# Kernel optimization log

Measured on AMD Instinct MI355X. Metric: run time of the kernel, lower is better.

Reference implementation:

```python
import jax, jax.numpy as jnp
import numpy as np

N = 100000   # nodes
E = 3200000  # edges
F = 128      # in = hidden = out channels
V = 8        # virtual nodes
L = 3        # conv layers
EPS = 1e-5


def setup_inputs() -> dict:
    key = jax.random.key(0)
    ks = jax.random.split(key, 16)
    rn = lambda k, s, sc=0.05: jax.random.normal(k, s, jnp.float32) * sc
    return {
        "x": rn(ks[0], (N, F), 1.0),
        "edge_index": jax.random.randint(ks[1], (2, E), 0, N, jnp.int32),
        "vn_mask": jax.random.randint(ks[2], (V, N), 0, 2, jnp.int32).astype(bool),
        "Wc": rn(ks[3], (L, F, F)),
        "bc": rn(ks[4], (L, F)),
        "bn_g": jnp.ones((L, F), jnp.float32),
        "bn_b": jnp.zeros((L, F), jnp.float32),
        "vn_embed": rn(ks[5], (V, F)),
        "mlp_W1": rn(ks[6], (L - 1, V, F, 2 * F)),
        "mlp_b1": rn(ks[7], (L - 1, V, 2 * F)),
        "ln1_g": jnp.ones((L - 1, V, 2 * F), jnp.float32),
        "ln1_b": jnp.zeros((L - 1, V, 2 * F), jnp.float32),
        "mlp_W2": rn(ks[8], (L - 1, V, 2 * F, F)),
        "mlp_b2": rn(ks[9], (L - 1, V, F)),
        "ln2_g": jnp.ones((L - 1, V, F), jnp.float32),
        "ln2_b": jnp.zeros((L - 1, V, F), jnp.float32),
    }


def _ln(h, g, b):
    m = h.mean(-1, keepdims=True)
    v = ((h - m) ** 2).mean(-1, keepdims=True)
    return (h - m) * jax.lax.rsqrt(v + EPS) * g + b


def _bn(h, g, b):  # training-mode batch stats over nodes (dropout p=0)
    m = h.mean(0)
    v = ((h - m) ** 2).mean(0)
    return (h - m) * jax.lax.rsqrt(v + EPS) * g + b


def reference(x, edge_index, vn_mask, Wc, bc, bn_g, bn_b, vn_embed,
              mlp_W1, mlp_b1, ln1_g, ln1_b, mlp_W2, mlp_b2, ln2_g, ln2_b):
    src, dst = edge_index[0], edge_index[1]
    loops = jnp.arange(N, dtype=src.dtype)
    src_f = jnp.concatenate([src, loops])   # GCN adds self-loops
    dst_f = jnp.concatenate([dst, loops])
    deg = jax.ops.segment_sum(jnp.ones(src_f.shape[0], x.dtype), dst_f, num_segments=N)
    dinv = jnp.where(deg > 0, jax.lax.rsqrt(deg), 0.0)
    norm = dinv[src_f] * dinv[dst_f]        # sym-normalized edge weights

    def gcn(h, W, b):  # PyG GCNConv: linear -> normalized scatter-sum -> bias
        hl = h @ W
        out = jax.ops.segment_sum(hl[src_f] * norm[:, None], dst_f, num_segments=N)
        return out + b

    maskf = vn_mask.astype(x.dtype)  # [V, N]
    vn = vn_embed                    # [V, F]
    embs = [x]
    for layer in range(L):
        h = embs[layer] + vn.sum(0, keepdims=True)       # aggregation='sum'
        h = gcn(h, Wc[layer], bc[layer])
        h = _bn(h, bn_g[layer], bn_b[layer])
        if layer != L - 1:
            h = jax.nn.relu(h)
        embs.append(h)
        if layer < L - 1:
            pooled = maskf @ embs[layer]                 # per-VN global_add_pool
            tmp = pooled + vn
            h1 = jax.nn.relu(jnp.einsum('vf,vfh->vh', tmp, mlp_W1[layer]) + mlp_b1[layer])
            h1 = _ln(h1, ln1_g[layer], ln1_b[layer])
            h2 = jax.nn.relu(jnp.einsum('vh,vhf->vf', h1, mlp_W2[layer]) + mlp_b2[layer])
            vn = _ln(h2, ln2_g[layer], ln2_b[layer])
    return embs[-1]  # JK='last'
```

## Files before the change

kernel.cpp:

```cpp
#include <hip/hip_runtime.h>
#include <hip/hip_bf16.h>
#include <hip/hip_fp16.h>

#define NN 100000
#define EE 3200000
#define FF 128
#define F2 256
#define VV 8
#define LL 3
#define EPSV 1e-5f
#define NB 98

static inline int idiv(int a, int b){ return (a + b - 1) / b; }

__global__ void k_deg(const int* __restrict__ dst, int* __restrict__ edeg){
  int stride = gridDim.x * 256;
  for (int e = blockIdx.x * 256 + threadIdx.x; e < EE; e += stride)
    atomicAdd(&edeg[dst[e]], 1);
}

__global__ void k_scanA(const int* __restrict__ edeg, int* __restrict__ offs,
                        int* __restrict__ bsum, float* __restrict__ dinv){
  __shared__ int s[1024];
  int t = threadIdx.x;
  int i = blockIdx.x * 1024 + t;
  int v = (i < NN) ? edeg[i] : 0;
  if (i < NN) dinv[i] = rsqrtf((float)(v + 1));
  int x = v;
  s[t] = x; __syncthreads();
  for (int d = 1; d < 1024; d <<= 1){
    int y = (t >= d) ? s[t - d] : 0;
    __syncthreads();
    x += y; s[t] = x;
    __syncthreads();
  }
  if (i < NN) offs[i] = x - v;
  if (t == 1023) bsum[blockIdx.x] = x;
}

__global__ void k_scanB(int* __restrict__ bsum){
  __shared__ int s[128];
  int t = threadIdx.x;
  s[t] = (t < NB) ? bsum[t] : 0;
  __syncthreads();
  if (t == 0){
    int run = 0;
    for (int k = 0; k < NB; ++k){ int tmp = s[k]; s[k] = run; run += tmp; }
  }
  __syncthreads();
  if (t < NB) bsum[t] = s[t];
}

__global__ void k_scanC(int* __restrict__ offs, const int* __restrict__ bsum,
                        int* __restrict__ cursor){
  int i = blockIdx.x * 256 + threadIdx.x;
  if (i < NN){
    int o = offs[i] + bsum[i >> 10];
    offs[i] = o;
    cursor[i] = o;
  }
  if (i == 0) offs[NN] = EE;
}

__global__ void k_scatter(const int* __restrict__ src, const int* __restrict__ dst,
                          int* __restrict__ cursor, int* __restrict__ ssorted){
  int stride = gridDim.x * 256;
  for (int e = blockIdx.x * 256 + threadIdx.x; e < EE; e += stride){
    int d = dst[e];
    int pos = atomicAdd(&cursor[d], 1);
    ssorted[pos] = src[e];
  }
}

__global__ void k_maskdetect(const unsigned char* __restrict__ m, int* __restrict__ flag){
  int any = 0;
  for (int t = threadIdx.x; t < 4096; t += 256)
    if ((t & 3) && m[t]) any = 1;
  if (any) atomicOr(flag, 1);
}

__launch_bounds__(256)
__global__ void k_matmul(const float* __restrict__ in, const float* __restrict__ W,
                         const float* __restrict__ vn, const float* __restrict__ dinv,
                         const float* __restrict__ ss, int hasbn,
                         uint2* __restrict__ hlb){
  __shared__ float Ws[FF * FF];
  __shared__ float As[32 * FF];
  __shared__ float vs[FF];
  __shared__ float rv[FF];
  __shared__ float scs[FF], shs[FF];
  int tid = threadIdx.x;
  for (int t = tid; t < FF * FF; t += 256) Ws[t] = W[t];
  if (tid < FF){
    float s = 0.f;
    for (int v = 0; v < VV; ++v) s += vn[v * FF + tid];
    vs[tid] = s;
    scs[tid] = hasbn ? ss[tid] : 1.0f;
    shs[tid] = hasbn ? ss[FF + tid] : 0.0f;
  }
  __syncthreads();
  if (tid < FF){
    float a = 0.f;
    for (int k = 0; k < FF; ++k) a += vs[k] * Ws[k * FF + tid];
    rv[tid] = a;
  }
  __syncthreads();
  int g = tid >> 5;
  int c = tid & 31;
  float4 rvv = ((const float4*)rv)[c];
  for (int base = blockIdx.x * 32; base < NN; base += gridDim.x * 32){
    const float4* in4 = (const float4*)(in + (size_t)base * FF);
    for (int i = tid; i < 32 * 32; i += 256){
      float4 vv = in4[i];
      if (hasbn){
        int cq = (i & 31) * 4;
        vv.x = fmaxf(fmaf(vv.x, scs[cq + 0], shs[cq + 0]), 0.f);
        vv.y = fmaxf(fmaf(vv.y, scs[cq + 1], shs[cq + 1]), 0.f);
        vv.z = fmaxf(fmaf(vv.z, scs[cq + 2], shs[cq + 2]), 0.f);
        vv.w = fmaxf(fmaf(vv.w, scs[cq + 3], shs[cq + 3]), 0.f);
      }
      ((float4*)As)[i] = vv;
    }
    __syncthreads();
    float4 a0 = rvv, a1 = rvv, a2 = rvv, a3 = rvv;
    #pragma unroll 4
    for (int k = 0; k < FF; ++k){
      float4 wv = ((const float4*)Ws)[k * 32 + c];
      float x0 = As[(g +  0) * FF + k];
      float x1 = As[(g +  8) * FF + k];
      float x2 = As[(g + 16) * FF + k];
      float x3 = As[(g + 24) * FF + k];
      a0.x += x0 * wv.x; a0.y += x0 * wv.y; a0.z += x0 * wv.z; a0.w += x0 * wv.w;
      a1.x += x1 * wv.x; a1.y += x1 * wv.y; a1.z += x1 * wv.z; a1.w += x1 * wv.w;
      a2.x += x2 * wv.x; a2.y += x2 * wv.y; a2.z += x2 * wv.z; a2.w += x2 * wv.w;
      a3.x += x3 * wv.x; a3.y += x3 * wv.y; a3.z += x3 * wv.z; a3.w += x3 * wv.w;
    }
    #pragma unroll
    for (int rr = 0; rr < 4; ++rr){
      float4 a = (rr == 0) ? a0 : (rr == 1) ? a1 : (rr == 2) ? a2 : a3;
      int r = base + g + 8 * rr;
      float d = dinv[r];
      __half2 h01 = __floats2half2_rn(a.x * d, a.y * d);
      __half2 h23 = __floats2half2_rn(a.z * d, a.w * d);
      uint2 pk;
      pk.x = *reinterpret_cast<unsigned int*>(&h01);
      pk.y = *reinterpret_cast<unsigned int*>(&h23);
      hlb[(size_t)r * 32 + c] = pk;
    }
    __syncthreads();
  }
}

__launch_bounds__(256)
__global__ void k_gather(const unsigned int* __restrict__ hlb, const float* __restrict__ dinv,
                         const int* __restrict__ offs, const int* __restrict__ ssorted,
                         float2* __restrict__ agg2, float* __restrict__ stats){
  int tid = threadIdx.x;
  int lane = tid & 63;
  int wid = (blockIdx.x * 256 + tid) >> 6;
  int nw = (gridDim.x * 256) >> 6;
  float s0 = 0.f, s1 = 0.f, q0 = 0.f, q1 = 0.f;
  for (int n = wid; n < NN; n += nw){
    int off0 = offs[n], off1 = offs[n + 1];
    unsigned int ps = hlb[(size_t)n * 64 + lane];
    float2 acc = __half22float2(*reinterpret_cast<__half2*>(&ps));
    #pragma unroll 8
    for (int e = off0; e < off1; ++e){
      unsigned int p = hlb[(size_t)ssorted[e] * 64 + lane];
      float2 f = __half22float2(*reinterpret_cast<__half2*>(&p));
      acc.x += f.x; acc.y += f.y;
    }
    float dv = dinv[n];
    float v0 = acc.x * dv, v1 = acc.y * dv;
    agg2[(size_t)n * 64 + lane] = make_float2(v0, v1);
    s0 += v0; s1 += v1; q0 += v0 * v0; q1 += v1 * v1;
  }
  __shared__ float4 red[256];
  red[tid] = make_float4(s0, s1, q0, q1);
  __syncthreads();
  if (tid < 64){
    float4 a = red[tid], b = red[tid + 64], c = red[tid + 128], d = red[tid + 192];
    a.x += b.x + c.x + d.x; a.y += b.y + c.y + d.y;
    a.z += b.z + c.z + d.z; a.w += b.w + c.w + d.w;
    atomicAdd(&stats[2 * tid], a.x);
    atomicAdd(&stats[2 * tid + 1], a.y);
    atomicAdd(&stats[FF + 2 * tid], a.z);
    atomicAdd(&stats[FF + 2 * tid + 1], a.w);
  }
}

__global__ void k_bnfin(const float* __restrict__ stats, const float* __restrict__ g,
                        const float* __restrict__ b, float* __restrict__ ss){
  int j = threadIdx.x;
  float mean = stats[j] * (1.0f / NN);
  float var  = stats[FF + j] * (1.0f / NN) - mean * mean;
  float sc = rsqrtf(var + EPSV) * g[j];
  ss[j] = sc;
  ss[FF + j] = b[j] - mean * sc;
}

__launch_bounds__(256)
__global__ void k_bnapply(float4* __restrict__ h, const float* __restrict__ stats,
                          const float* __restrict__ g, const float* __restrict__ b){
  __shared__ float ss[2 * FF];
  int tid = threadIdx.x;
  if (tid < FF){
    float mean = stats[tid] * (1.0f / NN);
    float var  = stats[FF + tid] * (1.0f / NN) - mean * mean;
    float sc = rsqrtf(var + EPSV) * g[tid];
    ss[tid] = sc;
    ss[FF + tid] = b[tid] - mean * sc;
  }
  __syncthreads();
  int n4 = NN * FF / 4;
  int stride = gridDim.x * 256;
  for (int i = blockIdx.x * 256 + tid; i < n4; i += stride){
    int c = (i & 31) * 4;
    float4 v = h[i];
    float4 sc = *(const float4*)&ss[c];
    float4 sh = *(const float4*)&ss[FF + c];
    v.x = v.x * sc.x + sh.x;
    v.y = v.y * sc.y + sh.y;
    v.z = v.z * sc.z + sh.z;
    v.w = v.w * sc.w + sh.w;
    h[i] = v;
  }
}

__global__ void k_pool(const float* __restrict__ emb, const unsigned char* __restrict__ m8,
                       const int* __restrict__ m32, const int* __restrict__ flag,
                       const float* __restrict__ ss, int hasbn,
                       float* __restrict__ pooled){
  int isb = *flag;
  int tid = blockIdx.x * 256 + threadIdx.x;
  int j = tid & 127;
  int r = tid >> 7;
  int rs = (gridDim.x * 256) >> 7;
  float sc = hasbn ? ss[j] : 1.0f;
  float sh = hasbn ? ss[FF + j] : 0.0f;
  float acc[VV];
  #pragma unroll
  for (int v = 0; v < VV; ++v) acc[v] = 0.f;
  for (; r < NN; r += rs){
    float xv = emb[r * FF + j];
    xv = fmaf(xv, sc, sh);
    if (hasbn) xv = fmaxf(xv, 0.f);
    #pragma unroll
    for (int v = 0; v < VV; ++v){
      int mv = isb ? (int)m8[v * NN + r] : m32[v * NN + r];
      if (mv) acc[v] += xv;
    }
  }
  #pragma unroll
  for (int v = 0; v < VV; ++v) atomicAdd(&pooled[v * FF + j], acc[v]);
}

__device__ __forceinline__ float blockSum(float x, float* red, int tid){
  red[tid] = x; __syncthreads();
  #pragma unroll
  for (int s = 128; s >= 1; s >>= 1){
    if (tid < s) red[tid] += red[tid + s];
    __syncthreads();
  }
  float r = red[0];
  __syncthreads();
  return r;
}

__launch_bounds__(256)
__global__ void k_vnmlp(const float* __restrict__ pooled, const float* __restrict__ vnin,
                        const float* __restrict__ W1, const float* __restrict__ b1,
                        const float* __restrict__ g1, const float* __restrict__ bb1,
                        const float* __restrict__ W2, const float* __restrict__ b2,
                        const float* __restrict__ g2, const float* __restrict__ bb2,
                        float* __restrict__ vnout){
  int v = blockIdx.x;
  int tid = threadIdx.x;
  __shared__ float tmp_s[FF];
  __shared__ float h1_s[F2];
  __shared__ float red[256];
  if (tid < FF) tmp_s[tid] = pooled[v * FF + tid] + vnin[v * FF + tid];
  __syncthreads();
  const float* W1v = W1 + (size_t)v * FF * F2;
  float acc = b1[v * F2 + tid];
  for (int k = 0; k < FF; ++k) acc += tmp_s[k] * W1v[k * F2 + tid];
  acc = fmaxf(acc, 0.f);
  float sum = blockSum(acc, red, tid);
  float sq  = blockSum(acc * acc, red, tid);
  float mean = sum * (1.f / F2);
  float var  = sq * (1.f / F2) - mean * mean;
  float y = (acc - mean) * rsqrtf(var + EPSV) * g1[v * F2 + tid] + bb1[v * F2 + tid];
  h1_s[tid] = y;
  __syncthreads();
  const float* W2v = W2 + (size_t)v * F2 * FF;
  float h2 = 0.f;
  if (tid < FF){
    float a2 = b2[v * FF + tid];
    for (int k = 0; k < F2; ++k) a2 += h1_s[k] * W2v[k * FF + tid];
    h2 = fmaxf(a2, 0.f);
  }
  float sum2 = blockSum((tid < FF) ? h2 : 0.f, red, tid);
  float sq2  = blockSum((tid < FF) ? h2 * h2 : 0.f, red, tid);
  float mean2 = sum2 * (1.f / FF);
  float var2  = sq2 * (1.f / FF) - mean2 * mean2;
  if (tid < FF)
    vnout[v * FF + tid] = (h2 - mean2) * rsqrtf(var2 + EPSV) * g2[v * FF + tid]
                          + bb2[v * FF + tid];
}

extern "C" void kernel_launch(void* const* d_in, const int* in_sizes, int n_in,
                              void* d_out, int out_size, void* d_ws, size_t ws_size,
                              hipStream_t stream){
  const float* x        = (const float*)d_in[0];
  const int*   ei       = (const int*)d_in[1];
  const unsigned char* vmask8 = (const unsigned char*)d_in[2];
  const int*   vmask32  = (const int*)d_in[2];
  const float* Wc       = (const float*)d_in[3];
  const float* bn_g     = (const float*)d_in[5];
  const float* bn_b     = (const float*)d_in[6];
  const float* vn_embed = (const float*)d_in[7];
  const float* mlp_W1   = (const float*)d_in[8];
  const float* mlp_b1   = (const float*)d_in[9];
  const float* ln1_g    = (const float*)d_in[10];
  const float* ln1_b    = (const float*)d_in[11];
  const float* mlp_W2   = (const float*)d_in[12];
  const float* mlp_b2   = (const float*)d_in[13];
  const float* ln2_g    = (const float*)d_in[14];
  const float* ln2_b    = (const float*)d_in[15];
  float* out = (float*)d_out;

  unsigned int* hlb = (unsigned int*)d_ws;
  float* bufB    = (float*)(hlb + (size_t)NN * 64);
  int*   ssorted = (int*)(bufB + (size_t)NN * FF);
  int*   offs    = ssorted + EE;
  int*   cursor  = offs + NN + 1;
  int*   edeg    = cursor + NN;
  int*   bsum    = edeg + NN;
  float* dinv    = (float*)(bsum + 128);
  float* stats   = dinv + NN;
  float* ssA     = stats + 2 * FF;
  float* ssB     = ssA + 2 * FF;
  float* pooled  = ssB + 2 * FF;
  float* vnA     = pooled + VV * FF;
  float* vnB     = vnA + VV * FF;
  int*   mflag   = (int*)(vnB + VV * FF);

  const int* esrc = ei;
  const int* edst = ei + EE;

  hipMemsetAsync(edeg, 0, NN * sizeof(int), stream);
  k_deg<<<1024, 256, 0, stream>>>(edst, edeg);
  k_scanA<<<NB, 1024, 0, stream>>>(edeg, offs, bsum, dinv);
  k_scanB<<<1, 128, 0, stream>>>(bsum);
  k_scanC<<<idiv(NN, 256), 256, 0, stream>>>(offs, bsum, cursor);
  k_scatter<<<2048, 256, 0, stream>>>(esrc, edst, cursor, ssorted);

  hipMemsetAsync(mflag, 0, sizeof(int), stream);
  k_maskdetect<<<1, 256, 0, stream>>>(vmask8, mflag);

  const float* vncur = vn_embed;
  const float* embin = x;
  float* ssbufs[2] = {ssA, ssB};
  const float* sscur = nullptr;
  float* vnbufs[2] = {vnA, vnB};

  for (int l = 0; l < LL; ++l){
    float* agg = (l < LL - 1) ? bufB : out;
    const float* Wl = Wc + (size_t)l * FF * FF;
    int hasbn = (l > 0) ? 1 : 0;

    k_matmul<<<1024, 256, 0, stream>>>(embin, Wl, vncur, dinv, sscur, hasbn, (uint2*)hlb);

    if (l < LL - 1){
      hipMemsetAsync(pooled, 0, VV * FF * sizeof(float), stream);
      k_pool<<<1024, 256, 0, stream>>>(embin, vmask8, vmask32, mflag, sscur, hasbn, pooled);
    }

    hipMemsetAsync(stats, 0, 2 * FF * sizeof(float), stream);
    k_gather<<<2048, 256, 0, stream>>>(hlb, dinv, offs, ssorted, (float2*)agg, stats);

    if (l < LL - 1){
      k_bnfin<<<1, 128, 0, stream>>>(stats, bn_g + l * FF, bn_b + l * FF, ssbufs[l]);
      k_vnmlp<<<VV, 256, 0, stream>>>(pooled, vncur,
          mlp_W1 + (size_t)l * VV * FF * F2, mlp_b1 + (size_t)l * VV * F2,
          ln1_g + (size_t)l * VV * F2, ln1_b + (size_t)l * VV * F2,
          mlp_W2 + (size_t)l * VV * F2 * FF, mlp_b2 + (size_t)l * VV * FF,
          ln2_g + (size_t)l * VV * FF, ln2_b + (size_t)l * VV * FF,
          vnbufs[l]);
      vncur = vnbufs[l];
      sscur = ssbufs[l];
      embin = agg;
    } else {
      k_bnapply<<<1024, 256, 0, stream>>>((float4*)out, stats, bn_g + l * FF, bn_b + l * FF);
    }
  }
}
```

Before: 1.666 ms.

## Partition CSR scatter by XCD destination slice and widen gather to half-wave per node

The scatter kernel now assigns each block to one of eight destination-node slices, chosen by block index modulo 8. Each block scans all edges but only inserts those whose destination falls in its slice, so a slice's cursor atomics and ssorted writes stay on one XCD's L2. The gather kernel now handles two nodes per wavefront, with 32 lanes each loading 8-byte fp16 quads, which gives wider loads and more nodes in flight. The cost is that every scatter group reads the full edge list, eight times the index traffic, and the XCD mapping assumes round-robin block dispatch.

```diff
diff --git a/kernel.cpp b/kernel.cpp
--- a/kernel.cpp
+++ b/kernel.cpp
@@ -10,6 +10,8 @@
 #define LL 3
 #define EPSV 1e-5f
 #define NB 98
+#define NXCD 8
+#define SLICE 12500
 
 static inline int idiv(int a, int b){ return (a + b - 1) / b; }
 
@@ -64,11 +66,17 @@
 
 __global__ void k_scatter(const int* __restrict__ src, const int* __restrict__ dst,
                           int* __restrict__ cursor, int* __restrict__ ssorted){
-  int stride = gridDim.x * 256;
-  for (int e = blockIdx.x * 256 + threadIdx.x; e < EE; e += stride){
+  int grp = blockIdx.x & (NXCD - 1);
+  int lo = grp * SLICE, hi = lo + SLICE;
+  int bid = blockIdx.x >> 3;
+  int nb = gridDim.x >> 3;
+  int stride = nb * 256;
+  for (int e = bid * 256 + threadIdx.x; e < EE; e += stride){
     int d = dst[e];
-    int pos = atomicAdd(&cursor[d], 1);
-    ssorted[pos] = src[e];
+    if (d >= lo && d < hi){
+      int pos = atomicAdd(&cursor[d], 1);
+      ssorted[pos] = src[e];
+    }
   }
 }
 
@@ -152,40 +160,53 @@
 }
 
 __launch_bounds__(256)
-__global__ void k_gather(const unsigned int* __restrict__ hlb, const float* __restrict__ dinv,
+__global__ void k_gather(const uint2* __restrict__ hlb2, const float* __restrict__ dinv,
                          const int* __restrict__ offs, const int* __restrict__ ssorted,
-                         float2* __restrict__ agg2, float* __restrict__ stats){
+                         float4* __restrict__ agg4, float* __restrict__ stats){
   int tid = threadIdx.x;
-  int lane = tid & 63;
-  int wid = (blockIdx.x * 256 + tid) >> 6;
-  int nw = (gridDim.x * 256) >> 6;
-  float s0 = 0.f, s1 = 0.f, q0 = 0.f, q1 = 0.f;
-  for (int n = wid; n < NN; n += nw){
+  int ln = tid & 31;
+  int half = (tid >> 5) & 1;
+  int pair = (blockIdx.x * 256 + tid) >> 6;
+  int np = (gridDim.x * 256) >> 6;
+  float s0=0.f,s1=0.f,s2=0.f,s3=0.f, q0=0.f,q1=0.f,q2=0.f,q3=0.f;
+  for (int p = pair; p < NN / 2; p += np){
+    int n = 2 * p + half;
     int off0 = offs[n], off1 = offs[n + 1];
-    unsigned int ps = hlb[(size_t)n * 64 + lane];
-    float2 acc = __half22float2(*reinterpret_cast<__half2*>(&ps));
+    uint2 u = hlb2[(size_t)n * 32 + ln];
+    float2 a01 = __half22float2(*reinterpret_cast<__half2*>(&u.x));
+    float2 a23 = __half22float2(*reinterpret_cast<__half2*>(&u.y));
+    float acc0 = a01.x, acc1 = a01.y, acc2 = a23.x, acc3 = a23.y;
     #pragma unroll 8
     for (int e = off0; e < off1; ++e){
-      unsigned int p = hlb[(size_t)ssorted[e] * 64 + lane];
-      float2 f = __half22float2(*reinterpret_cast<__half2*>(&p));
-      acc.x += f.x; acc.y += f.y;
+      uint2 v = hlb2[(size_t)ssorted[e] * 32 + ln];
+      float2 f01 = __half22float2(*reinterpret_cast<__half2*>(&v.x));
+      float2 f23 = __half22float2(*reinterpret_cast<__half2*>(&v.y));
+      acc0 += f01.x; acc1 += f01.y; acc2 += f23.x; acc3 += f23.y;
     }
     float dv = dinv[n];
-    float v0 = acc.x * dv, v1 = acc.y * dv;
-    agg2[(size_t)n * 64 + lane] = make_float2(v0, v1);
-    s0 += v0; s1 += v1; q0 += v0 * v0; q1 += v1 * v1;
-  }
-  __shared__ float4 red[256];
-  red[tid] = make_float4(s0, s1, q0, q1);
-  __syncthreads();
-  if (tid < 64){
-    float4 a = red[tid], b = red[tid + 64], c = red[tid + 128], d = red[tid + 192];
-    a.x += b.x + c.x + d.x; a.y += b.y + c.y + d.y;
-    a.z += b.z + c.z + d.z; a.w += b.w + c.w + d.w;
-    atomicAdd(&stats[2 * tid], a.x);
-    atomicAdd(&stats[2 * tid + 1], a.y);
-    atomicAdd(&stats[FF + 2 * tid], a.z);
-    atomicAdd(&stats[FF + 2 * tid + 1], a.w);
+    float v0 = acc0*dv, v1 = acc1*dv, v2 = acc2*dv, v3 = acc3*dv;
+    agg4[(size_t)n * 32 + ln] = make_float4(v0, v1, v2, v3);
+    s0 += v0; s1 += v1; s2 += v2; s3 += v3;
+    q0 += v0*v0; q1 += v1*v1; q2 += v2*v2; q3 += v3*v3;
+  }
+  __shared__ float sum_s[256][4];
+  __shared__ float sq_s[256][4];
+  sum_s[tid][0]=s0; sum_s[tid][1]=s1; sum_s[tid][2]=s2; sum_s[tid][3]=s3;
+  sq_s[tid][0]=q0; sq_s[tid][1]=q1; sq_s[tid][2]=q2; sq_s[tid][3]=q3;
+  __syncthreads();
+  if (tid < 32){
+    float ts[4] = {0,0,0,0}, tq[4] = {0,0,0,0};
+    #pragma unroll
+    for (int k = 0; k < 8; ++k){
+      int row = k * 32 + tid;
+      #pragma unroll
+      for (int c = 0; c < 4; ++c){ ts[c] += sum_s[row][c]; tq[c] += sq_s[row][c]; }
+    }
+    #pragma unroll
+    for (int c = 0; c < 4; ++c){
+      atomicAdd(&stats[4 * tid + c], ts[c]);
+      atomicAdd(&stats[FF + 4 * tid + c], tq[c]);
+    }
   }
 }
 
@@ -377,7 +398,8 @@
     }
 
     hipMemsetAsync(stats, 0, 2 * FF * sizeof(float), stream);
-    k_gather<<<2048, 256, 0, stream>>>(hlb, dinv, offs, ssorted, (float2*)agg, stats);
+    k_gather<<<2048, 256, 0, stream>>>((const uint2*)hlb, dinv, offs, ssorted,
+                                       (float4*)agg, stats);
 
     if (l < LL - 1){
       k_bnfin<<<1, 128, 0, stream>>>(stats, bn_g + l * FF, bn_b + l * FF, ssbufs[l]);
```

Result: slower. 1.798 ms (+7.9%).

## Chunk fp16 features by column and gather per chunk to fit cache

Applied to the files above, without the earlier changes.

The matmul now writes its half-precision output split into 8 column chunks of 16 features, each stored contiguously across all nodes. The gather kernel runs a 2D grid over node tiles and chunks, with eight lanes per node reading 32-byte slices, so each chunk's working set (about 3.2 MB) can stay in cache during random neighbor reads. BatchNorm statistics move out of the gather into a separate k_stats pass over the aggregated output. This adds one extra full read of the output and repeats the edge index reads once per chunk.

```diff
diff --git a/kernel.cpp b/kernel.cpp
--- a/kernel.cpp
+++ b/kernel.cpp
@@ -10,6 +10,8 @@
 #define LL 3
 #define EPSV 1e-5f
 #define NB 98
+#define NCHK 8
+#define NTIL 3125
 
 static inline int idiv(int a, int b){ return (a + b - 1) / b; }
 
@@ -107,6 +109,8 @@
   __syncthreads();
   int g = tid >> 5;
   int c = tid & 31;
+  int chk = c >> 2;
+  int cw  = c & 3;
   float4 rvv = ((const float4*)rv)[c];
   for (int base = blockIdx.x * 32; base < NN; base += gridDim.x * 32){
     const float4* in4 = (const float4*)(in + (size_t)base * FF);
@@ -145,7 +149,7 @@
       uint2 pk;
       pk.x = *reinterpret_cast<unsigned int*>(&h01);
       pk.y = *reinterpret_cast<unsigned int*>(&h23);
-      hlb[(size_t)r * 32 + c] = pk;
+      hlb[((size_t)chk * NN + r) * 4 + cw] = pk;
     }
     __syncthreads();
   }
@@ -154,38 +158,60 @@
 __launch_bounds__(256)
 __global__ void k_gather(const unsigned int* __restrict__ hlb, const float* __restrict__ dinv,
                          const int* __restrict__ offs, const int* __restrict__ ssorted,
-                         float2* __restrict__ agg2, float* __restrict__ stats){
+                         float2* __restrict__ agg2){
   int tid = threadIdx.x;
+  int w = tid >> 6;
   int lane = tid & 63;
-  int wid = (blockIdx.x * 256 + tid) >> 6;
-  int nw = (gridDim.x * 256) >> 6;
-  float s0 = 0.f, s1 = 0.f, q0 = 0.f, q1 = 0.f;
-  for (int n = wid; n < NN; n += nw){
-    int off0 = offs[n], off1 = offs[n + 1];
-    unsigned int ps = hlb[(size_t)n * 64 + lane];
-    float2 acc = __half22float2(*reinterpret_cast<__half2*>(&ps));
-    #pragma unroll 8
-    for (int e = off0; e < off1; ++e){
-      unsigned int p = hlb[(size_t)ssorted[e] * 64 + lane];
-      float2 f = __half22float2(*reinterpret_cast<__half2*>(&p));
-      acc.x += f.x; acc.y += f.y;
-    }
-    float dv = dinv[n];
-    float v0 = acc.x * dv, v1 = acc.y * dv;
-    agg2[(size_t)n * 64 + lane] = make_float2(v0, v1);
-    s0 += v0; s1 += v1; q0 += v0 * v0; q1 += v1 * v1;
-  }
-  __shared__ float4 red[256];
-  red[tid] = make_float4(s0, s1, q0, q1);
-  __syncthreads();
-  if (tid < 64){
-    float4 a = red[tid], b = red[tid + 64], c = red[tid + 128], d = red[tid + 192];
-    a.x += b.x + c.x + d.x; a.y += b.y + c.y + d.y;
-    a.z += b.z + c.z + d.z; a.w += b.w + c.w + d.w;
-    atomicAdd(&stats[2 * tid], a.x);
-    atomicAdd(&stats[2 * tid + 1], a.y);
-    atomicAdd(&stats[FF + 2 * tid], a.z);
-    atomicAdd(&stats[FF + 2 * tid + 1], a.w);
+  int sub = lane >> 3;
+  int word = lane & 7;
+  int c8 = blockIdx.y;
+  const unsigned int* hc = hlb + (size_t)c8 * NN * 8;
+  int n = blockIdx.x * 32 + (w << 3) + sub;
+  int off0 = offs[n], off1 = offs[n + 1];
+  unsigned int sv = hc[n * 8 + word];
+  float2 acc = __half22float2(*reinterpret_cast<__half2*>(&sv));
+  #pragma unroll 4
+  for (int e = off0; e < off1; ++e){
+    int s = ssorted[e];
+    unsigned int v = hc[s * 8 + word];
+    float2 f = __half22float2(*reinterpret_cast<__half2*>(&v));
+    acc.x += f.x; acc.y += f.y;
+  }
+  float dv = dinv[n];
+  agg2[(size_t)n * 64 + c8 * 8 + word] = make_float2(acc.x * dv, acc.y * dv);
+}
+
+__launch_bounds__(256)
+__global__ void k_stats(const float4* __restrict__ agg4, float* __restrict__ stats){
+  int tid = threadIdx.x;
+  int c = tid & 31;
+  int r = (blockIdx.x * 256 + tid) >> 5;
+  int rs = (gridDim.x * 256) >> 5;
+  float4 s = {0,0,0,0}, q = {0,0,0,0};
+  for (; r < NN; r += rs){
+    float4 v = agg4[(size_t)r * 32 + c];
+    s.x += v.x; s.y += v.y; s.z += v.z; s.w += v.w;
+    q.x += v.x*v.x; q.y += v.y*v.y; q.z += v.z*v.z; q.w += v.w*v.w;
+  }
+  __shared__ float4 sm[256], qm[256];
+  sm[tid] = s; qm[tid] = q;
+  __syncthreads();
+  if (tid < 32){
+    float4 ts = sm[tid], tq = qm[tid];
+    #pragma unroll
+    for (int k = 1; k < 8; ++k){
+      float4 a = sm[k * 32 + tid], b = qm[k * 32 + tid];
+      ts.x += a.x; ts.y += a.y; ts.z += a.z; ts.w += a.w;
+      tq.x += b.x; tq.y += b.y; tq.z += b.z; tq.w += b.w;
+    }
+    atomicAdd(&stats[4 * tid + 0], ts.x);
+    atomicAdd(&stats[4 * tid + 1], ts.y);
+    atomicAdd(&stats[4 * tid + 2], ts.z);
+    atomicAdd(&stats[4 * tid + 3], ts.w);
+    atomicAdd(&stats[FF + 4 * tid + 0], tq.x);
+    atomicAdd(&stats[FF + 4 * tid + 1], tq.y);
+    atomicAdd(&stats[FF + 4 * tid + 2], tq.z);
+    atomicAdd(&stats[FF + 4 * tid + 3], tq.w);
   }
 }
 
@@ -376,8 +402,10 @@
       k_pool<<<1024, 256, 0, stream>>>(embin, vmask8, vmask32, mflag, sscur, hasbn, pooled);
     }
 
+    k_gather<<<dim3(NTIL, NCHK), 256, 0, stream>>>(hlb, dinv, offs, ssorted, (float2*)agg);
+
     hipMemsetAsync(stats, 0, 2 * FF * sizeof(float), stream);
-    k_gather<<<2048, 256, 0, stream>>>(hlb, dinv, offs, ssorted, (float2*)agg, stats);
+    k_stats<<<1024, 256, 0, stream>>>((const float4*)agg, stats);
 
     if (l < LL - 1){
       k_bnfin<<<1, 128, 0, stream>>>(stats, bn_g + l * FF, bn_b + l * FF, ssbufs[l]);
```

Result: slower. 1.908 ms (+14.5%).

## Use fp16 MFMA for the per-layer node linear transform

Applied to the files above, without the earlier changes.

The node feature matmul now runs on matrix cores via 16x16x32 f16 MFMA instructions instead of scalar fp32 FMAs. Weight fragments are held in registers and input tiles are converted to fp16 in padded shared memory. Results are staged through a shared fp32 buffer before the dinv scaling and fp16 packing. The cost is that the inputs and weights are rounded to fp16 before the product, which lowers matmul precision, and each tile now has an extra shared-memory round trip.

```diff
diff --git a/kernel.cpp b/kernel.cpp
--- a/kernel.cpp
+++ b/kernel.cpp
@@ -10,6 +10,10 @@
 #define LL 3
 #define EPSV 1e-5f
 #define NB 98
+#define NTILES 3125
+
+typedef _Float16 f16x8 __attribute__((ext_vector_type(8)));
+typedef float f32x4 __attribute__((ext_vector_type(4)));
 
 static inline int idiv(int a, int b){ return (a + b - 1) / b; }
 
@@ -84,13 +88,10 @@
                          const float* __restrict__ vn, const float* __restrict__ dinv,
                          const float* __restrict__ ss, int hasbn,
                          uint2* __restrict__ hlb){
-  __shared__ float Ws[FF * FF];
-  __shared__ float As[32 * FF];
-  __shared__ float vs[FF];
-  __shared__ float rv[FF];
-  __shared__ float scs[FF], shs[FF];
-  int tid = threadIdx.x;
-  for (int t = tid; t < FF * FF; t += 256) Ws[t] = W[t];
+  __shared__ _Float16 As[32 * 136];
+  __shared__ float   Cs[32 * 132];
+  __shared__ float vs[FF], rv[FF], scs[FF], shs[FF];
+  int tid = threadIdx.x, lane = tid & 63, w = tid >> 6;
   if (tid < FF){
     float s = 0.f;
     for (int v = 0; v < VV; ++v) s += vn[v * FF + tid];
@@ -101,51 +102,79 @@
   __syncthreads();
   if (tid < FF){
     float a = 0.f;
-    for (int k = 0; k < FF; ++k) a += vs[k] * Ws[k * FF + tid];
+    for (int k = 0; k < FF; ++k) a += vs[k] * W[k * FF + tid];
     rv[tid] = a;
   }
-  __syncthreads();
-  int g = tid >> 5;
-  int c = tid & 31;
-  float4 rvv = ((const float4*)rv)[c];
-  for (int base = blockIdx.x * 32; base < NN; base += gridDim.x * 32){
-    const float4* in4 = (const float4*)(in + (size_t)base * FF);
+  f16x8 Bf[4][2];
+  int kg = (lane >> 4) * 8;
+  int cl = lane & 15;
+  #pragma unroll
+  for (int q = 0; q < 4; ++q)
+    #pragma unroll
+    for (int ct = 0; ct < 2; ++ct){
+      int col = (w * 2 + ct) * 16 + cl;
+      #pragma unroll
+      for (int j = 0; j < 8; ++j)
+        Bf[q][ct][j] = (_Float16)W[(q * 32 + kg + j) * FF + col];
+    }
+  __syncthreads();
+
+  for (int t = blockIdx.x; t < NTILES; t += gridDim.x){
+    int base = t * 32;
     for (int i = tid; i < 32 * 32; i += 256){
-      float4 vv = in4[i];
+      int r = i >> 5, cq = i & 31;
+      float4 v = ((const float4*)(in + (size_t)(base + r) * FF))[cq];
       if (hasbn){
-        int cq = (i & 31) * 4;
-        vv.x = fmaxf(fmaf(vv.x, scs[cq + 0], shs[cq + 0]), 0.f);
-        vv.y = fmaxf(fmaf(vv.y, scs[cq + 1], shs[cq + 1]), 0.f);
-        vv.z = fmaxf(fmaf(vv.z, scs[cq + 2], shs[cq + 2]), 0.f);
-        vv.w = fmaxf(fmaf(vv.w, scs[cq + 3], shs[cq + 3]), 0.f);
+        int c0 = cq * 4;
+        v.x = fmaxf(fmaf(v.x, scs[c0 + 0], shs[c0 + 0]), 0.f);
+        v.y = fmaxf(fmaf(v.y, scs[c0 + 1], shs[c0 + 1]), 0.f);
+        v.z = fmaxf(fmaf(v.z, scs[c0 + 2], shs[c0 + 2]), 0.f);
+        v.w = fmaxf(fmaf(v.w, scs[c0 + 3], shs[c0 + 3]), 0.f);
       }
-      ((float4*)As)[i] = vv;
-    }
-    __syncthreads();
-    float4 a0 = rvv, a1 = rvv, a2 = rvv, a3 = rvv;
-    #pragma unroll 4
-    for (int k = 0; k < FF; ++k){
-      float4 wv = ((const float4*)Ws)[k * 32 + c];
-      float x0 = As[(g +  0) * FF + k];
-      float x1 = As[(g +  8) * FF + k];
-      float x2 = As[(g + 16) * FF + k];
-      float x3 = As[(g + 24) * FF + k];
-      a0.x += x0 * wv.x; a0.y += x0 * wv.y; a0.z += x0 * wv.z; a0.w += x0 * wv.w;
-      a1.x += x1 * wv.x; a1.y += x1 * wv.y; a1.z += x1 * wv.z; a1.w += x1 * wv.w;
-      a2.x += x2 * wv.x; a2.y += x2 * wv.y; a2.z += x2 * wv.z; a2.w += x2 * wv.w;
-      a3.x += x3 * wv.x; a3.y += x3 * wv.y; a3.z += x3 * wv.z; a3.w += x3 * wv.w;
-    }
+      _Float16* ap = &As[r * 136 + cq * 4];
+      ap[0] = (_Float16)v.x; ap[1] = (_Float16)v.y;
+      ap[2] = (_Float16)v.z; ap[3] = (_Float16)v.w;
+    }
+    __syncthreads();
+    f32x4 acc[2][2] = {{{0,0,0,0},{0,0,0,0}},{{0,0,0,0},{0,0,0,0}}};
     #pragma unroll
-    for (int rr = 0; rr < 4; ++rr){
-      float4 a = (rr == 0) ? a0 : (rr == 1) ? a1 : (rr == 2) ? a2 : a3;
-      int r = base + g + 8 * rr;
-      float d = dinv[r];
-      __half2 h01 = __floats2half2_rn(a.x * d, a.y * d);
-      __half2 h23 = __floats2half2_rn(a.z * d, a.w * d);
+    for (int q = 0; q < 4; ++q){
+      f16x8 Af[2];
+      #pragma unroll
+      for (int rt = 0; rt < 2; ++rt)
+        Af[rt] = *(const f16x8*)&As[(rt * 16 + cl) * 136 + q * 32 + kg];
+      #pragma unroll
+      for (int rt = 0; rt < 2; ++rt)
+        #pragma unroll
+        for (int ct = 0; ct < 2; ++ct)
+          acc[rt][ct] = __builtin_amdgcn_mfma_f32_16x16x32_f16(Af[rt], Bf[q][ct], acc[rt][ct], 0, 0, 0);
+    }
+    #pragma unroll
+    for (int rt = 0; rt < 2; ++rt)
+      #pragma unroll
+      for (int ct = 0; ct < 2; ++ct){
+        int col = (w * 2 + ct) * 16 + cl;
+        int r0 = rt * 16 + (lane >> 4) * 4;
+        #pragma unroll
+        for (int reg = 0; reg < 4; ++reg)
+          Cs[(r0 + reg) * 132 + col] = acc[rt][ct][reg];
+      }
+    __syncthreads();
+    for (int i = tid; i < 32 * 32; i += 256){
+      int r = i >> 5, cq = i & 31;
+      float d = dinv[base + r];
+      float4 c = *(const float4*)&Cs[r * 132 + cq * 4];
+      int c0 = cq * 4;
+      float a0 = (c.x + rv[c0 + 0]) * d;
+      float a1 = (c.y + rv[c0 + 1]) * d;
+      float a2 = (c.z + rv[c0 + 2]) * d;
+      float a3 = (c.w + rv[c0 + 3]) * d;
+      __half2 h01 = __floats2half2_rn(a0, a1);
+      __half2 h23 = __floats2half2_rn(a2, a3);
       uint2 pk;
       pk.x = *reinterpret_cast<unsigned int*>(&h01);
       pk.y = *reinterpret_cast<unsigned int*>(&h23);
-      hlb[(size_t)r * 32 + c] = pk;
+      hlb[(size_t)(base + r) * 32 + cq] = pk;
     }
     __syncthreads();
   }
```

Result: faster. 1.442 ms (-13.4%).
